# Kernel optimization log

Measured on AMD Instinct MI355X. Metric: run time of the kernel, lower is better.

Reference implementation:

```python
import jax, jax.numpy as jnp
import numpy as np

IMG = 14          # image_x_y_dim
STRIDE = 4        # stride == kernel_size == n_qubits
H_MAT = jnp.array([[1.0, 1.0], [1.0, -1.0]], dtype=jnp.complex64) / np.sqrt(2.0)
_RZ_SIGNS = jnp.array([-0.5j, 0.5j], dtype=jnp.complex64)


def _apply_1q(state, U, w):
    # contract 2x2 gate U into wire-axis w of state with shape (2,)*n
    s = jnp.tensordot(U, state, axes=[[1], [w]])
    return jnp.moveaxis(s, 0, w)


def _rz(state, theta, w, n):
    d = jnp.exp(_RZ_SIGNS * theta)  # diag(e^{-i t/2}, e^{i t/2})
    shape = [1] * n
    shape[w] = 2
    return state * d.reshape(shape)


def _rx(state, theta, w):
    c = jnp.cos(0.5 * theta).astype(jnp.complex64)
    s = ((-1j) * jnp.sin(0.5 * theta)).astype(jnp.complex64)
    U = jnp.stack([jnp.stack([c, s]), jnp.stack([s, c])])
    return _apply_1q(state, U, w)


def _ry(state, theta, w):
    c = jnp.cos(0.5 * theta).astype(jnp.complex64)
    s = jnp.sin(0.5 * theta).astype(jnp.complex64)
    U = jnp.stack([jnp.stack([c, -s]), jnp.stack([s, c])])
    return _apply_1q(state, U, w)


def _crz(state, theta, cw, tw, n):
    # PennyLane CRZ: diag(1, 1, e^{-i t/2}, e^{i t/2}) in |control, target> basis
    d = jnp.exp(_RZ_SIGNS * theta)
    P = jnp.stack([jnp.ones(2, jnp.complex64), d])  # axes: (control, target)
    if cw > tw:
        P = P.T
    a, b = min(cw, tw), max(cw, tw)
    shape = [1] * n
    shape[a] = 2
    shape[b] = 2
    return state * P.reshape(shape)


def _zexp(state, n):
    probs = state.real ** 2 + state.imag ** 2
    outs = []
    for w in range(n):
        shape = [1] * n
        shape[w] = 2
        sgn = jnp.array([1.0, -1.0], jnp.float32).reshape(shape)
        outs.append(jnp.sum(probs * sgn))
    return jnp.stack(outs)  # (n,)


def _circuit4(x, weights):
    # x: (L,) with L in {4, 8, 16}; weights: (2, 8)
    n, vpq, L = 4, 4, x.shape[0]
    state = jnp.zeros((2,) * n, jnp.complex64).at[(0,) * n].set(1.0)
    for q in range(n):  # encoding: H then alternating RZ/RX per qubit
        state = _apply_1q(state, H_MAT, q)
        for i in range(vpq):
            idx = q * vpq + i
            if idx < L:
                state = _rz(state, x[idx], q, n) if i % 2 == 0 else _rx(state, x[idx], q)
    for l in range(2):  # n_layers
        for i in range(n):
            state = _crz(state, weights[l, i], i, (i + 1) % n, n)
        for j in range(n, 2 * n):
            state = _ry(state, weights[l, j], j % n)
    return _zexp(state, n)  # (4,)


def _circuit8(x, weights):
    # x: (64,); weights: (3, 16); angles scaled by pi as in qnn_circuit
    n, L = 8, 64
    vpq = L // n + 1  # 9
    state = jnp.zeros((2,) * n, jnp.complex64).at[(0,) * n].set(1.0)
    for q in range(n):
        state = _apply_1q(state, H_MAT, q)
        for i in range(vpq):
            idx = q * vpq + i
            if idx < L:
                theta = np.pi * x[idx]
                state = _rz(state, theta, q, n) if i % 2 == 0 else _rx(state, theta, q)
    for l in range(3):  # qnn_layers
        for i in range(n):
            state = _crz(state, weights[l, i], i, (i + 1) % n, n)
        for j in range(n, 2 * n):
            state = _ry(state, weights[l, j], j % n)
    return _zexp(state, n)  # (8,)


def _forward_single(x196, w1, w2, fc_w, fc_b):
    img = x196.reshape(IMG, IMG)
    feats = []
    for i in range(0, IMG, STRIDE):
        for j in range(0, IMG, STRIDE):
            patch = img[i:i + 4, j:j + 4].reshape(-1)  # edge patches truncate to 8 or 4
            feats.append(_circuit4(patch, w1))
    f = jnp.concatenate(feats)       # (64,)
    g = _circuit8(f, w2)             # (8,)
    return fc_w @ g + fc_b           # (3,)


def setup_inputs() -> dict:
    key = jax.random.key(0)
    k0, k1, k2, k3, k4 = jax.random.split(key, 5)
    bs = 8192
    X = jax.random.normal(k0, (bs, 196), jnp.float32)
    w1 = jax.random.uniform(k1, (2, 8), jnp.float32, 0.0, 2.0 * np.pi)
    w2 = jax.random.uniform(k2, (3, 16), jnp.float32, 0.0, 2.0 * np.pi)
    fc_w = jax.random.normal(k3, (3, 8), jnp.float32) / np.sqrt(8.0)
    fc_b = jax.random.normal(k4, (3,), jnp.float32) * 0.01
    return {"X": X, "w1": w1, "w2": w2, "fc_w": fc_w, "fc_b": fc_b}


def reference(X, w1, w2, fc_w, fc_b):
    return jax.vmap(_forward_single, in_axes=(0, None, None, None, None))(X, w1, w2, fc_w, fc_b)
```

## Files before the change

kernel.cpp:

```cpp
#include <hip/hip_runtime.h>

#define DEV __device__ __forceinline__

namespace {

typedef float f32x2 __attribute__((ext_vector_type(2)));

DEV f32x2 splat(float x){ f32x2 r; r.x = x; r.y = x; return r; }
DEV f32x2 csw(f32x2 a){ return __builtin_shufflevector(a, a, 1, 0); }
DEV f32x2 cmulv(f32x2 a, f32x2 b){
  f32x2 nt; nt.x = -b.y; nt.y = b.x;
  return splat(a.x)*b + splat(a.y)*nt;
}
DEV f32x2 cconj(f32x2 a){ a.y = -a.y; return a; }
DEV f32x2 cphase2(f32x2 a, float c, float s){
  f32x2 sv; sv.x = -s; sv.y = s;
  return splat(c)*a + sv*csw(a);
}
DEV void halfsc(float th, float& c, float& s){ __sincosf(0.5f*th, &s, &c); }

constexpr float RSQRT2 = 0.70710678118654752440f;
constexpr float PI_F   = 3.14159265358979323846f;

template<int CTRL> DEV float qperm(float v){
  return __int_as_float(__builtin_amdgcn_mov_dpp(__float_as_int(v), CTRL, 0xF, 0xF, true));
}
template<int OFF> DEV float swzf(float v){
  return __int_as_float(__builtin_amdgcn_ds_swizzle(__float_as_int(v), OFF));
}
template<int B> DEV float shfx(float v){
  if constexpr (B==1)      return qperm<0xB1>(v);
  else if constexpr (B==2) return qperm<0x4E>(v);
  else if constexpr (B==4) return swzf<0x101F>(v);
  else                     return qperm<0x128>(v);
}

template<int I0, int N> DEV void run_gates(f32x2 (&v)[2], const float* f, float scale){
  #pragma unroll
  for (int i = I0; i < I0 + N; ++i){
    float c, s; halfsc(scale * f[i], c, s);
    f32x2 cv = splat(c);
    f32x2 sp; sp.x = s;  sp.y = -s;
    if ((i & 1) == 0){
      f32x2 sn; sn.x = -s; sn.y = s;
      v[0] = cv*v[0] + sp*csw(v[0]);
      v[1] = cv*v[1] + sn*csw(v[1]);
    } else {
      f32x2 t0 = csw(v[0]), t1 = csw(v[1]);
      v[0] = cv*v[0] + sp*t1;
      v[1] = cv*v[1] + sp*t0;
    }
  }
}
template<int N> DEV void build_psi(f32x2 (&v)[2], const float* ang, float scale){
  v[0].x = RSQRT2; v[0].y = 0.f;
  v[1].x = RSQRT2; v[1].y = 0.f;
  run_gates<0, N>(v, ang, scale);
}

template<int S> DEV void ry_loc16(f32x2 (&a)[16], float2 cs){
  const float c = cs.x, s = cs.y;
  #pragma unroll
  for (int m = 0; m < 16; ++m) if (!(m & S)) {
    f32x2 u = a[m], v = a[m|S];
    a[m]   = splat(c)*u - splat(s)*v;
    a[m|S] = splat(s)*u + splat(c)*v;
  }
}
template<int MASK> DEV void ry_lane16(f32x2 (&a)[16], int r, float2 cs){
  const float c = cs.x;
  const float sg = (r & MASK) ? cs.y : -cs.y;
  #pragma unroll
  for (int m = 0; m < 16; ++m){
    f32x2 o; o.x = shfx<MASK>(a[m].x); o.y = shfx<MASK>(a[m].y);
    a[m] = splat(c)*a[m] + splat(sg)*o;
  }
}

DEV f32x2 tov(float2 v){ f32x2 r; r.x = v.x; r.y = v.y; return r; }

}

__global__ __launch_bounds__(256, 2)
void qnn_fused_kernel(const float* __restrict__ X,  const float* __restrict__ w1,
                      const float* __restrict__ w2, const float* __restrict__ fcw,
                      const float* __restrict__ fcb, float* __restrict__ out, int bs)
{
  __shared__ float  feats[16][80];
  __shared__ float4 p1chain[16][16][5];
  __shared__ float4 chainH[16][8][2];
  __shared__ float4 chain2[16][9];
  __shared__ float2 p1phi2[2][16];
  __shared__ float2 p1ry[2][4];
  __shared__ float2 ryw[3][8];
  __shared__ float2 phi2[3*16*18];

  const int t  = threadIdx.x;
  const int sl = t >> 4;
  const int r  = t & 15;
  int sample = blockIdx.x * 16 + sl;
  if (sample >= bs) sample = bs - 1;

  if (t < 32){
    const int l = t >> 4, m = t & 15;
    const float h0 = 0.5f*w1[l*8+0], h1 = 0.5f*w1[l*8+1];
    const float h2 = 0.5f*w1[l*8+2], h3 = 0.5f*w1[l*8+3];
    const bool b0 = m & 8, b1 = m & 4, b2 = m & 2, b3 = m & 1;
    float phi = 0.f;
    phi += b0 ? (b1 ? h0 : -h0) : 0.f;
    phi += b1 ? (b2 ? h1 : -h1) : 0.f;
    phi += b2 ? (b3 ? h2 : -h2) : 0.f;
    phi += b3 ? (b0 ? h3 : -h3) : 0.f;
    float c, s; __sincosf(phi, &s, &c);
    p1phi2[l][m] = {c, s};
  } else if (t < 40){
    const int j = t - 32, l = j >> 2, i = j & 3;
    float c, s; halfsc(w1[l*8 + 4 + i], c, s); p1ry[l][i] = {c, s};
  } else if (t < 64){
    const int j = t - 40, l = j >> 3, i = j & 7;
    float c, s; halfsc(w2[l*16 + 8 + i], c, s); ryw[l][i] = {c, s};
  }
  #pragma unroll
  for (int jj = 0; jj < 3; ++jj){
    const int idx = t + jj*256;
    const int l = idx >> 8, rr = (idx >> 4) & 15, mm = idx & 15;
    const float* wl = w2 + l*16;
    float h[8];
    #pragma unroll
    for (int i = 0; i < 8; ++i) h[i] = 0.5f*wl[i];
    bool b[8];
    b[0]=(rr>>3)&1; b[1]=(rr>>2)&1; b[2]=(rr>>1)&1; b[3]=rr&1;
    b[4]=(mm>>3)&1; b[5]=(mm>>2)&1; b[6]=(mm>>1)&1; b[7]=mm&1;
    float phi = 0.f;
    #pragma unroll
    for (int i = 0; i < 8; ++i)
      phi += b[i] ? (b[(i+1)&7] ? h[i] : -h[i]) : 0.f;
    float c, s; __sincosf(phi, &s, &c);
    phi2[(l*16 + rr)*18 + mm] = {c, s};
  }

  #pragma unroll
  for (int jj = 0; jj < 4; ++jj){
    const int j = t + jj*256;
    const int s_ = j >> 6, p = (j >> 2) & 15, q = j & 3;
    const int pi = p >> 2, pj = p & 3;
    const int shift = (pj == 3) ? 1 : 2;
    const int cmask = (1 << shift) - 1;
    const int limit = ((pi == 3) ? 2 : 4) << shift;
    int gs = blockIdx.x * 16 + s_;
    if (gs >= bs) gs = bs - 1;
    const float* Xf = X + (size_t)gs * 196;
    float ang[4];
    #pragma unroll
    for (int i = 0; i < 4; ++i){
      const int k = q*4 + i;
      int idx = (pi*4 + (k >> shift))*14 + pj*4 + (k & cmask);
      idx = idx > 195 ? 195 : idx;
      float v = Xf[idx];
      ang[i] = (k < limit) ? v : 0.f;
    }
    f32x2 v[2];
    build_psi<4>(v, ang, 1.0f);
    p1chain[s_][p][q] = {v[0].x, v[0].y, v[1].x, v[1].y};
  }
  __syncthreads();

  {
    f32x2 ps[4][2];
    #pragma unroll
    for (int q = 0; q < 4; ++q){
      float4 fq = p1chain[sl][r][q];
      ps[q][0].x = fq.x; ps[q][0].y = fq.y;
      ps[q][1].x = fq.z; ps[q][1].y = fq.w;
    }
    f32x2 a[16];
    {
      f32x2 T01[4], T23[4];
      #pragma unroll
      for (int j = 0; j < 4; ++j){
        T01[j] = cmulv(ps[0][j>>1], ps[1][j&1]);
        T23[j] = cmulv(ps[2][j>>1], ps[3][j&1]);
      }
      #pragma unroll
      for (int m = 0; m < 16; ++m) a[m] = cmulv(T01[m>>2], T23[m&3]);
    }

    #pragma unroll
    for (int l = 0; l < 2; ++l){
      const float4* ph4 = (const float4*)&p1phi2[l][0];
      #pragma unroll
      for (int j = 0; j < 8; ++j){
        float4 w = ph4[j];
        a[2*j]   = cphase2(a[2*j],   w.x, w.y);
        a[2*j+1] = cphase2(a[2*j+1], w.z, w.w);
      }
      ry_loc16<8>(a, p1ry[l][0]); ry_loc16<4>(a, p1ry[l][1]);
      ry_loc16<2>(a, p1ry[l][2]); ry_loc16<1>(a, p1ry[l][3]);
    }

    float pr[16];
    #pragma unroll
    for (int m = 0; m < 16; ++m) pr[m] = a[m].x*a[m].x + a[m].y*a[m].y;
    #pragma unroll
    for (int w = 0; w < 4; ++w){
      const int S = 8 >> w;
      float e = 0.f;
      #pragma unroll
      for (int m = 0; m < 16; ++m) e += (m & S) ? -pr[m] : pr[m];
      feats[sl][r*4 + w] = e;
    }
    feats[sl][64 + r] = 0.f;
  }
  __syncthreads();

  {
    const int h = t >> 7, idx = t & 127;
    const int s_ = idx >> 3, c = idx & 7;
    const float* f = &feats[s_][c*9];
    f32x2 v[2];
    if (h == 0){
      build_psi<5>(v, f, PI_F);
    } else {
      v[0].x = 1.f; v[0].y = 0.f;
      v[1].x = 0.f; v[1].y = 0.f;
      run_gates<5, 4>(v, f, PI_F);
    }
    chainH[s_][c][h] = {v[0].x, v[0].y, v[1].x, v[1].y};
  }
  __syncthreads();
  if (t < 128){
    const int s_ = t >> 3, c = t & 7;
    float4 A = chainH[s_][c][0], B = chainH[s_][c][1];
    f32x2 vA0, vA1, al, be;
    vA0.x=A.x; vA0.y=A.y; vA1.x=A.z; vA1.y=A.w;
    al.x=B.x;  al.y=B.y;  be.x=B.z;  be.y=B.w;
    f32x2 v0 = cmulv(al, vA0) - cmulv(cconj(be), vA1);
    f32x2 v1 = cmulv(be, vA0) + cmulv(cconj(al), vA1);
    chain2[s_][c] = {v0.x, v0.y, v1.x, v1.y};
  }
  __syncthreads();

  f32x2 a[16];
  {
    const float2* c2 = (const float2*)&chain2[sl][0];
    f32x2 e0 = tov(c2[0*2 + ((r>>3)&1)]);
    f32x2 e1 = tov(c2[1*2 + ((r>>2)&1)]);
    f32x2 e2 = tov(c2[2*2 + ((r>>1)&1)]);
    f32x2 e3 = tov(c2[3*2 + ( r    &1)]);
    f32x2 L  = cmulv(cmulv(e0, e1), cmulv(e2, e3));

    float4 q4 = chain2[sl][4], q5 = chain2[sl][5];
    float4 q6 = chain2[sl][6], q7 = chain2[sl][7];
    f32x2 p4[2], p5[2], p6[2], p7[2];
    p4[0].x=q4.x; p4[0].y=q4.y; p4[1].x=q4.z; p4[1].y=q4.w;
    p5[0].x=q5.x; p5[0].y=q5.y; p5[1].x=q5.z; p5[1].y=q5.w;
    p6[0].x=q6.x; p6[0].y=q6.y; p6[1].x=q6.z; p6[1].y=q6.w;
    p7[0].x=q7.x; p7[0].y=q7.y; p7[1].x=q7.z; p7[1].y=q7.w;
    f32x2 p45[4], p67[4];
    #pragma unroll
    for (int j = 0; j < 4; ++j){
      p45[j] = cmulv(p4[j>>1], p5[j&1]);
      p67[j] = cmulv(p6[j>>1], p7[j&1]);
    }
    f32x2 Lp[4];
    #pragma unroll
    for (int j = 0; j < 4; ++j) Lp[j] = cmulv(L, p45[j]);
    #pragma unroll
    for (int m = 0; m < 16; ++m) a[m] = cmulv(Lp[m>>2], p67[m&3]);
  }

  #pragma unroll
  for (int l = 0; l < 3; ++l){
    const float4* ph4 = (const float4*)&phi2[(l*16 + r)*18];
    #pragma unroll
    for (int j = 0; j < 8; ++j){
      float4 w = ph4[j];
      a[2*j]   = cphase2(a[2*j],   w.x, w.y);
      a[2*j+1] = cphase2(a[2*j+1], w.z, w.w);
    }
    ry_lane16<8>(a, r, ryw[l][0]);
    ry_lane16<4>(a, r, ryw[l][1]);
    ry_lane16<2>(a, r, ryw[l][2]);
    ry_lane16<1>(a, r, ryw[l][3]);
    ry_loc16<8>(a, ryw[l][4]);
    ry_loc16<4>(a, ryw[l][5]);
    ry_loc16<2>(a, ryw[l][6]);
    ry_loc16<1>(a, ryw[l][7]);
  }

  float pr[16];
  #pragma unroll
  for (int m = 0; m < 16; ++m) pr[m] = a[m].x*a[m].x + a[m].y*a[m].y;
  float Ssum = 0.f;
  #pragma unroll
  for (int m = 0; m < 16; ++m) Ssum += pr[m];
  float gp[8];
  gp[0] = (r & 8) ? -Ssum : Ssum;
  gp[1] = (r & 4) ? -Ssum : Ssum;
  gp[2] = (r & 2) ? -Ssum : Ssum;
  gp[3] = (r & 1) ? -Ssum : Ssum;
  #pragma unroll
  for (int w = 4; w < 8; ++w){
    const int S = 8 >> (w-4);
    float e = 0.f;
    #pragma unroll
    for (int m = 0; m < 16; ++m) e += (m & S) ? -pr[m] : pr[m];
    gp[w] = e;
  }

  float o0 = 0.f, o1 = 0.f, o2 = 0.f;
  #pragma unroll
  for (int w = 0; w < 8; ++w){
    o0 += fcw[0*8 + w] * gp[w];
    o1 += fcw[1*8 + w] * gp[w];
    o2 += fcw[2*8 + w] * gp[w];
  }
  o0 += shfx<1>(o0); o1 += shfx<1>(o1); o2 += shfx<1>(o2);
  o0 += shfx<2>(o0); o1 += shfx<2>(o1); o2 += shfx<2>(o2);
  o0 += shfx<4>(o0); o1 += shfx<4>(o1); o2 += shfx<4>(o2);
  o0 += shfx<8>(o0); o1 += shfx<8>(o1); o2 += shfx<8>(o2);

  if (r < 3){
    float o = (r == 0) ? o0 : ((r == 1) ? o1 : o2);
    out[(size_t)sample*3 + r] = o + fcb[r];
  }
}

extern "C" void kernel_launch(void* const* d_in, const int* in_sizes, int n_in,
                              void* d_out, int out_size, void* d_ws, size_t ws_size,
                              hipStream_t stream)
{
  const float* X   = (const float*)d_in[0];
  const float* w1  = (const float*)d_in[1];
  const float* w2  = (const float*)d_in[2];
  const float* fcw = (const float*)d_in[3];
  const float* fcb = (const float*)d_in[4];
  float* out = (float*)d_out;
  const int bs = in_sizes[0] / 196;
  const int blocks = (bs + 15) / 16;
  hipLaunchKernelGGL(qnn_fused_kernel, dim3(blocks), dim3(256), 0, stream,
                     X, w1, w2, fcw, fcb, out, bs);
}
```

Baseline: 17.05 us.

## Remap samples per wavefront and replace block barriers with wave-local LDS fences

The patch-chain build loop now assigns four samples to each wavefront, so everything a sample needs is produced and consumed inside one wave. That lets two of the block-wide __syncthreads be replaced by s_waitcnt lgkmcnt(0) fences. The two-half chain split (build_psi<5> plus run_gates, then a combining SU(2) product through chainH) is collapsed into one build_psi<9> per chain on 32 lanes. This removes barriers and an LDS round trip, but serializes nine gates per lane and leaves half of each wave idle in that stage. It also relies on in-wave lockstep for LDS visibility.

```diff
diff --git a/kernel.cpp b/kernel.cpp
--- a/kernel.cpp
+++ b/kernel.cpp
@@ -12,7 +12,6 @@
   f32x2 nt; nt.x = -b.y; nt.y = b.x;
   return splat(a.x)*b + splat(a.y)*nt;
 }
-DEV f32x2 cconj(f32x2 a){ a.y = -a.y; return a; }
 DEV f32x2 cphase2(f32x2 a, float c, float s){
   f32x2 sv; sv.x = -s; sv.y = s;
   return splat(c)*a + sv*csw(a);
@@ -21,6 +20,8 @@
 
 constexpr float RSQRT2 = 0.70710678118654752440f;
 constexpr float PI_F   = 3.14159265358979323846f;
+
+DEV void wave_lds_fence(){ asm volatile("s_waitcnt lgkmcnt(0)" ::: "memory"); }
 
 template<int CTRL> DEV float qperm(float v){
   return __int_as_float(__builtin_amdgcn_mov_dpp(__float_as_int(v), CTRL, 0xF, 0xF, true));
@@ -88,7 +89,6 @@
 {
   __shared__ float  feats[16][80];
   __shared__ float4 p1chain[16][16][5];
-  __shared__ float4 chainH[16][8][2];
   __shared__ float4 chain2[16][9];
   __shared__ float2 p1phi2[2][16];
   __shared__ float2 p1ry[2][4];
@@ -96,6 +96,8 @@
   __shared__ float2 phi2[3*16*18];
 
   const int t  = threadIdx.x;
+  const int wv = t >> 6;
+  const int ln = t & 63;
   const int sl = t >> 4;
   const int r  = t & 15;
   int sample = blockIdx.x * 16 + sl;
@@ -140,9 +142,9 @@
   }
 
   #pragma unroll
-  for (int jj = 0; jj < 4; ++jj){
-    const int j = t + jj*256;
-    const int s_ = j >> 6, p = (j >> 2) & 15, q = j & 3;
+  for (int k = 0; k < 4; ++k){
+    const int s_ = wv*4 + k;
+    const int p = ln >> 2, q = ln & 3;
     const int pi = p >> 2, pj = p & 3;
     const int shift = (pj == 3) ? 1 : 2;
     const int cmask = (1 << shift) - 1;
@@ -153,11 +155,11 @@
     float ang[4];
     #pragma unroll
     for (int i = 0; i < 4; ++i){
-      const int k = q*4 + i;
-      int idx = (pi*4 + (k >> shift))*14 + pj*4 + (k & cmask);
+      const int k2 = q*4 + i;
+      int idx = (pi*4 + (k2 >> shift))*14 + pj*4 + (k2 & cmask);
       idx = idx > 195 ? 195 : idx;
       float v = Xf[idx];
-      ang[i] = (k < limit) ? v : 0.f;
+      ang[i] = (k2 < limit) ? v : 0.f;
     }
     f32x2 v[2];
     build_psi<4>(v, ang, 1.0f);
@@ -211,34 +213,15 @@
     }
     feats[sl][64 + r] = 0.f;
   }
-  __syncthreads();
-
-  {
-    const int h = t >> 7, idx = t & 127;
-    const int s_ = idx >> 3, c = idx & 7;
-    const float* f = &feats[s_][c*9];
+  wave_lds_fence();
+
+  if (ln < 32){
+    const int s_ = wv*4 + (ln >> 3), c = ln & 7;
     f32x2 v[2];
-    if (h == 0){
-      build_psi<5>(v, f, PI_F);
-    } else {
-      v[0].x = 1.f; v[0].y = 0.f;
-      v[1].x = 0.f; v[1].y = 0.f;
-      run_gates<5, 4>(v, f, PI_F);
-    }
-    chainH[s_][c][h] = {v[0].x, v[0].y, v[1].x, v[1].y};
-  }
-  __syncthreads();
-  if (t < 128){
-    const int s_ = t >> 3, c = t & 7;
-    float4 A = chainH[s_][c][0], B = chainH[s_][c][1];
-    f32x2 vA0, vA1, al, be;
-    vA0.x=A.x; vA0.y=A.y; vA1.x=A.z; vA1.y=A.w;
-    al.x=B.x;  al.y=B.y;  be.x=B.z;  be.y=B.w;
-    f32x2 v0 = cmulv(al, vA0) - cmulv(cconj(be), vA1);
-    f32x2 v1 = cmulv(be, vA0) + cmulv(cconj(al), vA1);
-    chain2[s_][c] = {v0.x, v0.y, v1.x, v1.y};
-  }
-  __syncthreads();
+    build_psi<9>(v, &feats[s_][c*9], PI_F);
+    chain2[s_][c] = {v[0].x, v[0].y, v[1].x, v[1].y};
+  }
+  wave_lds_fence();
 
   f32x2 a[16];
   {
```

Result: no change. 17.02 us (median of 2 runs) (-0.2%).

## Build patch states in registers and replace block barriers with wave-local LDS fences

Applied to the files above, without the earlier changes.

Each thread now loads its own 16 patch pixels and builds the four per-qubit encoded states in registers, so the p1chain shared-memory round trip and its redistribution go away. The stage-2 work mapping is reassigned so each wavefront handles only the 4 samples it produced. That lets three __syncthreads be replaced with s_waitcnt lgkmcnt(0) fences that only wait for the wave's own LDS operations. The cost is that each thread computes more encoding gates (redundant work is spread differently). Correctness now depends on wave64 lockstep semantics and on the compiler not reordering LDS accesses across the asm fence.

```diff
diff --git a/kernel.cpp b/kernel.cpp
--- a/kernel.cpp
+++ b/kernel.cpp
@@ -21,6 +21,8 @@
 
 constexpr float RSQRT2 = 0.70710678118654752440f;
 constexpr float PI_F   = 3.14159265358979323846f;
+
+DEV void wave_lds_fence(){ asm volatile("s_waitcnt lgkmcnt(0)" ::: "memory"); }
 
 template<int CTRL> DEV float qperm(float v){
   return __int_as_float(__builtin_amdgcn_mov_dpp(__float_as_int(v), CTRL, 0xF, 0xF, true));
@@ -87,7 +89,6 @@
                       const float* __restrict__ fcb, float* __restrict__ out, int bs)
 {
   __shared__ float  feats[16][80];
-  __shared__ float4 p1chain[16][16][5];
   __shared__ float4 chainH[16][8][2];
   __shared__ float4 chain2[16][9];
   __shared__ float2 p1phi2[2][16];
@@ -96,6 +97,8 @@
   __shared__ float2 phi2[3*16*18];
 
   const int t  = threadIdx.x;
+  const int wv = t >> 6;
+  const int ln = t & 63;
   const int sl = t >> 4;
   const int r  = t & 15;
   int sample = blockIdx.x * 16 + sl;
@@ -139,40 +142,27 @@
     phi2[(l*16 + rr)*18 + mm] = {c, s};
   }
 
-  #pragma unroll
-  for (int jj = 0; jj < 4; ++jj){
-    const int j = t + jj*256;
-    const int s_ = j >> 6, p = (j >> 2) & 15, q = j & 3;
-    const int pi = p >> 2, pj = p & 3;
+  f32x2 ps[4][2];
+  {
+    const int pi = r >> 2, pj = r & 3;
     const int shift = (pj == 3) ? 1 : 2;
     const int cmask = (1 << shift) - 1;
     const int limit = ((pi == 3) ? 2 : 4) << shift;
-    int gs = blockIdx.x * 16 + s_;
-    if (gs >= bs) gs = bs - 1;
-    const float* Xf = X + (size_t)gs * 196;
-    float ang[4];
-    #pragma unroll
-    for (int i = 0; i < 4; ++i){
-      const int k = q*4 + i;
+    const float* Xf = X + (size_t)sample * 196;
+    float px[16];
+    #pragma unroll
+    for (int k = 0; k < 16; ++k){
       int idx = (pi*4 + (k >> shift))*14 + pj*4 + (k & cmask);
       idx = idx > 195 ? 195 : idx;
       float v = Xf[idx];
-      ang[i] = (k < limit) ? v : 0.f;
-    }
-    f32x2 v[2];
-    build_psi<4>(v, ang, 1.0f);
-    p1chain[s_][p][q] = {v[0].x, v[0].y, v[1].x, v[1].y};
+      px[k] = (k < limit) ? v : 0.f;
+    }
+    #pragma unroll
+    for (int q = 0; q < 4; ++q) build_psi<4>(ps[q], &px[q*4], 1.0f);
   }
   __syncthreads();
 
   {
-    f32x2 ps[4][2];
-    #pragma unroll
-    for (int q = 0; q < 4; ++q){
-      float4 fq = p1chain[sl][r][q];
-      ps[q][0].x = fq.x; ps[q][0].y = fq.y;
-      ps[q][1].x = fq.z; ps[q][1].y = fq.w;
-    }
     f32x2 a[16];
     {
       f32x2 T01[4], T23[4];
@@ -211,11 +201,11 @@
     }
     feats[sl][64 + r] = 0.f;
   }
-  __syncthreads();
+  wave_lds_fence();
 
   {
-    const int h = t >> 7, idx = t & 127;
-    const int s_ = idx >> 3, c = idx & 7;
+    const int h = ln >> 5, idx = ln & 31;
+    const int s_ = wv*4 + (idx >> 3), c = idx & 7;
     const float* f = &feats[s_][c*9];
     f32x2 v[2];
     if (h == 0){
@@ -227,9 +217,9 @@
     }
     chainH[s_][c][h] = {v[0].x, v[0].y, v[1].x, v[1].y};
   }
-  __syncthreads();
-  if (t < 128){
-    const int s_ = t >> 3, c = t & 7;
+  wave_lds_fence();
+  if (ln < 32){
+    const int s_ = wv*4 + (ln >> 3), c = ln & 7;
     float4 A = chainH[s_][c][0], B = chainH[s_][c][1];
     f32x2 vA0, vA1, al, be;
     vA0.x=A.x; vA0.y=A.y; vA1.x=A.z; vA1.y=A.w;
@@ -238,7 +228,7 @@
     f32x2 v1 = cmulv(be, vA0) + cmulv(cconj(al), vA1);
     chain2[s_][c] = {v0.x, v0.y, v1.x, v1.y};
   }
-  __syncthreads();
+  wave_lds_fence();
 
   f32x2 a[16];
   {
```

Result: no change. 17.38 us (+1.9%).
